# Performance work log

Measured on AMD Instinct MI355X. Metric: run time of the kernel, lower is better.

The kernel has to match this reference:

```python
import jax, jax.numpy as jnp
import numpy as np

K_NN = 32          # configs['k']
LEAKY_ALPHA = 0.2  # configs['alpha']
NHEADS = 8         # all heads share gat_W0/gat_a0 in the weights dict -> tiled output
NEG_INF = -9e15    # masked-softmax fill used by dense GAT


@jax.custom_vjp
def grad_reverse(x):
    # GradientReversalLayer: identity forward, negated gradient backward
    return x

def _gr_fwd(x):
    return x, None

def _gr_bwd(res, g):
    return (-g,)

grad_reverse.defvjp(_gr_fwd, _gr_bwd)


def setup_inputs() -> dict:
    key = jax.random.key(0)
    ks = jax.random.split(key, 11)
    N, D = 6144, 512           # N = (num_domains+1)*batch_size = 4*1536
    H1, H2, G = 256, 128, 64   # hidden_layers=[256,128], gat_hidden=[64]
    C, ND = 16, 3              # num_classes, num source-domain discriminators

    def xav(k, shape):
        limit = np.float32(np.sqrt(6.0 / (shape[0] + shape[1])) * 1.414)
        return jax.random.uniform(k, shape, jnp.float32, -limit, limit)

    return {
        "x": jax.random.normal(ks[0], (N, D), jnp.float32),
        "fc_W0": xav(ks[1], (D, H1)),
        "fc_b0": jax.random.normal(ks[2], (H1,), jnp.float32) * 0.01,
        "fc_W1": xav(ks[3], (H1, H2)),
        "fc_b1": jax.random.normal(ks[4], (H2,), jnp.float32) * 0.01,
        "gat_W": xav(ks[5], (H2, G)),
        "gat_a": jax.random.normal(ks[6], (2 * G, 1), jnp.float32) * 0.1,
        "cls_W": xav(ks[7], (NHEADS * G, C)),
        "cls_b": jax.random.normal(ks[8], (C,), jnp.float32) * 0.01,
        "dsc_W": jax.random.uniform(ks[9], (ND, NHEADS * G, 2), jnp.float32),
        "dsc_b": jax.random.uniform(ks[10], (ND, 2), jnp.float32),
    }


def reference(x, fc_W0, fc_b0, fc_W1, fc_b1, gat_W, gat_a, cls_W, cls_b, dsc_W, dsc_b):
    # --- feature extractor MLP (Linear 'fc' + relu), dropout=0 / eval mode ---
    h = jax.nn.relu(x @ fc_W0 + fc_b0)
    h = jax.nn.relu(h @ fc_W1 + fc_b1)          # [N, 128]
    n = h.shape[0]

    # --- AdjacencyLayer / DistanceLayer: kNN over pairwise L2 distances ---
    sq = jnp.sum(h * h, axis=1)
    d2 = sq[:, None] + sq[None, :] - 2.0 * (h @ h.T)      # [N, N] squared dists
    d2 = d2 + jnp.eye(n, dtype=h.dtype) * 1e9             # exclude self from kNN
    _, idx = jax.lax.top_k(-jax.lax.stop_gradient(d2), K_NN)  # [N, K]
    adj = jnp.zeros((n, n), h.dtype).at[jnp.arange(n)[:, None], idx].set(1.0)
    adj = adj + jnp.eye(n, dtype=h.dtype)                 # self loops

    # --- dense GraphAttentionLayer (single shared head, tiled nheads times) ---
    Wh = h @ gat_W                                        # [N, G]
    Gd = Wh.shape[1]
    f1 = Wh @ gat_a[:Gd]                                  # [N, 1]
    f2 = Wh @ gat_a[Gd:]                                  # [N, 1]
    e = jax.nn.leaky_relu(f1 + f2.T, LEAKY_ALPHA)         # [N, N]
    att = jax.nn.softmax(jnp.where(adj > 0, e, NEG_INF), axis=1)
    hp = jax.nn.elu(att @ Wh)                             # [N, G]
    gat_out = jnp.tile(hp, (1, NHEADS))                   # concat of shared heads

    # --- class head + domain discriminators behind gradient reversal ---
    cls_logits = gat_out @ cls_W + cls_b                  # [N, C]
    rev = grad_reverse(gat_out)
    dsc_logits = jnp.einsum('nd,kdo->nko', rev, dsc_W) + dsc_b  # [N, ND, 2]
    return jnp.concatenate([cls_logits, dsc_logits.reshape(n, -1)], axis=1)
```

## Files before the change

kernel.cpp:

```cpp
#include <hip/hip_runtime.h>
#include <float.h>

#define N_PTS 6144
#define D_IN  512
#define H1_DIM 256
#define H2_DIM 128
#define G_DIM  64
#define KNN    32
#define NOUT   22
#define NQ     (N_PTS / 4)

typedef short s8v __attribute__((ext_vector_type(8)));
typedef float f32x4 __attribute__((ext_vector_type(4)));
typedef unsigned u32x4 __attribute__((ext_vector_type(4)));
typedef unsigned short u16;
typedef unsigned short u16x4 __attribute__((ext_vector_type(4)));
typedef unsigned long long u64;

__device__ __forceinline__ u16 f2bf(float f) {
  unsigned u = __float_as_uint(f);
  u += 0x7FFFu + ((u >> 16) & 1u);
  return (u16)(u >> 16);
}
__device__ __forceinline__ float bf2f(u16 s) {
  return __uint_as_float(((unsigned)s) << 16);
}
__device__ __forceinline__ void split3(float v, u16& a0, u16& a1, u16& a2) {
  a0 = f2bf(v);
  float r1 = v - bf2f(a0);
  a1 = f2bf(r1);
  a2 = f2bf(r1 - bf2f(a1));
}
__device__ __forceinline__ unsigned sortkey(float f) {
  unsigned ub = __float_as_uint(f);
  return (ub & 0x80000000u) ? ~ub : (ub | 0x80000000u);
}

template<int BM, bool AF32, bool SPLITK, bool BIAS, bool RELU, bool WF32, bool WSPLIT>
__global__ __launch_bounds__(256, 4) void mfma_gemm(
    const void* __restrict__ A0any, const u16* __restrict__ A1_, const u16* __restrict__ A2_,
    const u16* __restrict__ B0_, const u16* __restrict__ B1_, const u16* __restrict__ B2_,
    const float* __restrict__ bias,
    float* __restrict__ Cf, u16* __restrict__ C0, u16* __restrict__ C1, u16* __restrict__ C2,
    int Ktot, int Ks, int ldC, size_t MN)
{
  const int MT = BM / 32, NT = 2;
  const int APL = BM * 32;
  const int BBASE = 3 * APL;
  __shared__ u16 lds[(BM + 64) * 32 * 3];

  const int t = threadIdx.x;
  const int lane = t & 63, wave = t >> 6;
  const int wm = wave >> 1, wn = wave & 1;
  const int m0 = blockIdx.y * BM, n0 = blockIdx.x * 64;
  const int kz = blockIdx.z * Ks;

  f32x4 acc[MT][NT] = {};

  const int pA = BM / 16;
  const int NC = 3 * pA + 12;

  for (int k0 = 0; k0 < Ks; k0 += 32) {
    if (k0) __syncthreads();
    const int kb = kz + k0;
    if (AF32) {
      const float* A = (const float*)A0any;
      #pragma unroll
      for (int c0 = 0; c0 < BM * 4; c0 += 256) {
        int c = c0 + t;
        int row = c >> 2, slot = c & 3;
        const float* g = A + (size_t)(m0 + row) * Ktot + kb + slot * 8;
        f32x4 fa = *(const f32x4*)g;
        f32x4 fb = *(const f32x4*)(g + 4);
        int dst = row * 32 + ((slot ^ ((row >> 1) & 3)) << 3);
        s8v v0, v1, v2;
        #pragma unroll
        for (int e = 0; e < 4; ++e) {
          u16 a0, a1, a2; split3(fa[e], a0, a1, a2);
          v0[e] = (short)a0; v1[e] = (short)a1; v2[e] = (short)a2;
        }
        #pragma unroll
        for (int e = 0; e < 4; ++e) {
          u16 a0, a1, a2; split3(fb[e], a0, a1, a2);
          v0[4 + e] = (short)a0; v1[4 + e] = (short)a1; v2[4 + e] = (short)a2;
        }
        *(s8v*)(lds + dst) = v0;
        *(s8v*)(lds + APL + dst) = v1;
        *(s8v*)(lds + 2 * APL + dst) = v2;
      }
      for (int c = wave; c < 12; c += 4) {
        int p = c >> 2, lc = c & 3;
        int row = lc * 16 + (lane >> 2);
        int srcslot = (lane & 3) ^ ((row >> 1) & 3);
        const u16* src = (p == 0) ? B0_ : (p == 1) ? B1_ : B2_;
        const u16* g = src + (size_t)(n0 + row) * Ktot + kb + srcslot * 8;
        __builtin_amdgcn_global_load_lds(
            (const __attribute__((address_space(1))) unsigned*)g,
            (__attribute__((address_space(3))) unsigned*)(lds + BBASE + p * 2048 + lc * 512),
            16, 0, 0);
      }
    } else {
      for (int c = wave; c < NC; c += 4) {
        const u16* src; int dstoff; int row0; int lc;
        if (c < 3 * pA) {
          int p = c / pA; lc = c % pA;
          src = (p == 0) ? (const u16*)A0any : (p == 1) ? A1_ : A2_;
          dstoff = p * APL + lc * 512;
          row0 = m0;
        } else {
          int cb = c - 3 * pA;
          int p = cb >> 2; lc = cb & 3;
          src = (p == 0) ? B0_ : (p == 1) ? B1_ : B2_;
          dstoff = BBASE + p * 2048 + lc * 512;
          row0 = n0;
        }
        int row = lc * 16 + (lane >> 2);
        int srcslot = (lane & 3) ^ ((row >> 1) & 3);
        const u16* g = src + (size_t)(row0 + row) * Ktot + kb + srcslot * 8;
        __builtin_amdgcn_global_load_lds(
            (const __attribute__((address_space(1))) unsigned*)g,
            (__attribute__((address_space(3))) unsigned*)(lds + dstoff),
            16, 0, 0);
      }
    }
    __syncthreads();

    s8v af[3][MT], bf[3][NT];
    #pragma unroll
    for (int mt = 0; mt < MT; ++mt) {
      int r = wm * (BM / 2) + mt * 16 + (lane & 15);
      int off = r * 32 + (((lane >> 4) ^ ((r >> 1) & 3)) << 3);
      #pragma unroll
      for (int p = 0; p < 3; ++p) af[p][mt] = *(const s8v*)(lds + p * APL + off);
    }
    #pragma unroll
    for (int nt = 0; nt < NT; ++nt) {
      int r = wn * 32 + nt * 16 + (lane & 15);
      int off = r * 32 + (((lane >> 4) ^ ((r >> 1) & 3)) << 3);
      #pragma unroll
      for (int p = 0; p < 3; ++p) bf[p][nt] = *(const s8v*)(lds + BBASE + p * 2048 + off);
    }
    #pragma unroll
    for (int mt = 0; mt < MT; ++mt)
      #pragma unroll
      for (int nt = 0; nt < NT; ++nt) {
        f32x4 a = acc[mt][nt];
        a = __builtin_amdgcn_mfma_f32_16x16x32_bf16(af[0][mt], bf[0][nt], a, 0, 0, 0);
        a = __builtin_amdgcn_mfma_f32_16x16x32_bf16(af[0][mt], bf[1][nt], a, 0, 0, 0);
        a = __builtin_amdgcn_mfma_f32_16x16x32_bf16(af[1][mt], bf[0][nt], a, 0, 0, 0);
        a = __builtin_amdgcn_mfma_f32_16x16x32_bf16(af[1][mt], bf[1][nt], a, 0, 0, 0);
        a = __builtin_amdgcn_mfma_f32_16x16x32_bf16(af[0][mt], bf[2][nt], a, 0, 0, 0);
        a = __builtin_amdgcn_mfma_f32_16x16x32_bf16(af[2][mt], bf[0][nt], a, 0, 0, 0);
        acc[mt][nt] = a;
      }
  }

  #pragma unroll
  for (int mt = 0; mt < MT; ++mt) {
    #pragma unroll
    for (int nt = 0; nt < NT; ++nt) {
      int col = n0 + wn * 32 + nt * 16 + (lane & 15);
      float bv = (BIAS && !SPLITK) ? bias[col] : 0.f;
      #pragma unroll
      for (int v = 0; v < 4; ++v) {
        int row = m0 + wm * (BM / 2) + mt * 16 + (lane >> 4) * 4 + v;
        float val = acc[mt][nt][v] + bv;
        size_t o = (size_t)row * ldC + col;
        if (SPLITK) {
          Cf[(size_t)blockIdx.z * MN + o] = val;
        } else {
          if (RELU) val = fmaxf(val, 0.f);
          if (WF32) Cf[o] = val;
          if (WSPLIT) {
            u16 a0, a1, a2; split3(val, a0, a1, a2);
            C0[o] = a0; C1[o] = a1; C2[o] = a2;
          }
        }
      }
    }
  }
}

__global__ __launch_bounds__(512, 4) void gram_symm(
    const u16* __restrict__ A0, const u16* __restrict__ A1, const u16* __restrict__ A2,
    const float* __restrict__ sq, u16* __restrict__ Ck, u16* __restrict__ Qm, int ldC)
{
  if ((int)blockIdx.x < (int)blockIdx.y) return;
  const int MT = 4, NT = 2;
  __shared__ u16 lds[2 * 128 * 32 * 3];

  const int t = threadIdx.x;
  const int lane = t & 63, wave = t >> 6;
  const int wm = wave >> 2, wn = wave & 3;
  const int m0 = blockIdx.y * 128, n0 = blockIdx.x * 128;
  const bool mirror = (int)blockIdx.x > (int)blockIdx.y;

  f32x4 acc[MT][NT] = {};

  for (int k0 = 0; k0 < H2_DIM; k0 += 32) {
    if (k0) __syncthreads();
    for (int c = wave; c < 48; c += 8) {
      int half = c >= 24;
      int cb = half ? c - 24 : c;
      int p = cb >> 3, lc = cb & 7;
      const u16* src = (p == 0) ? A0 : (p == 1) ? A1 : A2;
      int dstoff = half * 12288 + p * 4096 + lc * 512;
      int row0 = half ? n0 : m0;
      int row = lc * 16 + (lane >> 2);
      int srcslot = (lane & 3) ^ ((row >> 1) & 3);
      const u16* g = src + (size_t)(row0 + row) * H2_DIM + k0 + srcslot * 8;
      __builtin_amdgcn_global_load_lds(
          (const __attribute__((address_space(1))) unsigned*)g,
          (__attribute__((address_space(3))) unsigned*)(lds + dstoff),
          16, 0, 0);
    }
    __syncthreads();

    s8v af[3][MT], bf[3][NT];
    #pragma unroll
    for (int mt = 0; mt < MT; ++mt) {
      int r = wm * 64 + mt * 16 + (lane & 15);
      int off = r * 32 + (((lane >> 4) ^ ((r >> 1) & 3)) << 3);
      #pragma unroll
      for (int p = 0; p < 3; ++p) af[p][mt] = *(const s8v*)(lds + p * 4096 + off);
    }
    #pragma unroll
    for (int nt = 0; nt < NT; ++nt) {
      int r = wn * 32 + nt * 16 + (lane & 15);
      int off = r * 32 + (((lane >> 4) ^ ((r >> 1) & 3)) << 3);
      #pragma unroll
      for (int p = 0; p < 3; ++p) bf[p][nt] = *(const s8v*)(lds + 12288 + p * 4096 + off);
    }
    #pragma unroll
    for (int mt = 0; mt < MT; ++mt)
      #pragma unroll
      for (int nt = 0; nt < NT; ++nt) {
        f32x4 a = acc[mt][nt];
        a = __builtin_amdgcn_mfma_f32_16x16x32_bf16(af[0][mt], bf[0][nt], a, 0, 0, 0);
        a = __builtin_amdgcn_mfma_f32_16x16x32_bf16(af[0][mt], bf[1][nt], a, 0, 0, 0);
        a = __builtin_amdgcn_mfma_f32_16x16x32_bf16(af[1][mt], bf[0][nt], a, 0, 0, 0);
        a = __builtin_amdgcn_mfma_f32_16x16x32_bf16(af[1][mt], bf[1][nt], a, 0, 0, 0);
        a = __builtin_amdgcn_mfma_f32_16x16x32_bf16(af[0][mt], bf[2][nt], a, 0, 0, 0);
        a = __builtin_amdgcn_mfma_f32_16x16x32_bf16(af[2][mt], bf[0][nt], a, 0, 0, 0);
        acc[mt][nt] = a;
      }
  }

  unsigned mk32[MT][NT][2];
  __syncthreads();
  u16* stD = lds;
  #pragma unroll
  for (int mt = 0; mt < MT; ++mt) {
    #pragma unroll
    for (int nt = 0; nt < NT; ++nt) {
      int cl = wn * 32 + nt * 16 + (lane & 15);
      float sqc = sq[n0 + cl];
      #pragma unroll
      for (int v = 0; v < 4; ++v) {
        int rl = wm * 64 + mt * 16 + (lane >> 4) * 4 + v;
        float val = acc[mt][nt][v];
        float f = fmaf(-2.f, val, sqc);
        unsigned uu = sortkey(f);
        if (m0 + rl == n0 + cl) uu = 0xFFFFFFFFu;
        stD[rl * 136 + cl] = (u16)(uu >> 16);
        if (mirror) {
          unsigned km = sortkey(fmaf(-2.f, val, sq[m0 + rl])) >> 16;
          if (v & 1) mk32[mt][nt][v >> 1] |= km << 16;
          else       mk32[mt][nt][v >> 1] = km;
        }
      }
    }
  }
  __syncthreads();
  for (int e = t; e < 128 * 16; e += 512) {
    int row = e >> 4, ch = e & 15;
    u32x4 vv = *(const u32x4*)(stD + row * 136 + ch * 8);
    *(u32x4*)(Ck + (size_t)(m0 + row) * ldC + n0 + ch * 8) = vv;
  }
  for (int e = t; e < 128 * 32; e += 512) {
    int row = e >> 5, qg = e & 31;
    const u16* p = stD + row * 136 + qg * 4;
    u16 a = p[0] < p[1] ? p[0] : p[1];
    u16 b = p[2] < p[3] ? p[2] : p[3];
    Qm[(size_t)(m0 + row) * NQ + (n0 >> 2) + qg] = a < b ? a : b;
  }
  if (mirror) {
    __syncthreads();
    u16* stM = lds;
    #pragma unroll
    for (int mt = 0; mt < MT; ++mt) {
      #pragma unroll
      for (int nt = 0; nt < NT; ++nt) {
        int cl = wn * 32 + nt * 16 + (lane & 15);
        #pragma unroll
        for (int v = 0; v < 4; ++v) {
          int rl = wm * 64 + mt * 16 + (lane >> 4) * 4 + v;
          unsigned km = (v & 1) ? (mk32[mt][nt][v >> 1] >> 16)
                                : (mk32[mt][nt][v >> 1] & 0xFFFFu);
          stM[cl * 136 + rl] = (u16)km;
        }
      }
    }
    __syncthreads();
    for (int e = t; e < 128 * 16; e += 512) {
      int row = e >> 4, ch = e & 15;
      u32x4 vv = *(const u32x4*)(stM + row * 136 + ch * 8);
      *(u32x4*)(Ck + (size_t)(n0 + row) * ldC + m0 + ch * 8) = vv;
    }
    for (int e = t; e < 128 * 32; e += 512) {
      int row = e >> 5, qg = e & 31;
      const u16* p = stM + row * 136 + qg * 4;
      u16 a = p[0] < p[1] ? p[0] : p[1];
      u16 b = p[2] < p[3] ? p[2] : p[3];
      Qm[(size_t)(n0 + row) * NQ + (m0 >> 2) + qg] = a < b ? a : b;
    }
  }
}

template<int S, bool BIAS, bool RELU, bool WF32, bool WSPLIT>
__global__ void combine(const float* __restrict__ P, const float* __restrict__ bias,
                        size_t MN, int Ncols,
                        float* __restrict__ Cf, u16* __restrict__ C0,
                        u16* __restrict__ C1, u16* __restrict__ C2)
{
  size_t idx = ((size_t)blockIdx.x * 256 + threadIdx.x) * 4;
  if (idx >= MN) return;
  f32x4 s = *(const f32x4*)(P + idx);
  #pragma unroll
  for (int z = 1; z < S; ++z) s += *(const f32x4*)(P + (size_t)z * MN + idx);
  int n = (int)(idx % (size_t)Ncols);
  #pragma unroll
  for (int e = 0; e < 4; ++e) {
    float v = s[e] + (BIAS ? bias[n + e] : 0.f);
    if (RELU) v = fmaxf(v, 0.f);
    if (WF32) Cf[idx + e] = v;
    if (WSPLIT) {
      u16 a0, a1, a2; split3(v, a0, a1, a2);
      C0[idx + e] = a0; C1[idx + e] = a1; C2[idx + e] = a2;
    }
  }
}

__global__ void prep_all(const float* __restrict__ W0, u16* __restrict__ a0,
                         u16* __restrict__ a1, u16* __restrict__ a2,
                         const float* __restrict__ W1, u16* __restrict__ b0,
                         u16* __restrict__ b1, u16* __restrict__ b2,
                         const float* __restrict__ gW, u16* __restrict__ c0,
                         u16* __restrict__ c1, u16* __restrict__ c2,
                         const float* __restrict__ cW, const float* __restrict__ cb,
                         const float* __restrict__ dW, const float* __restrict__ db,
                         float* __restrict__ Wc, float* __restrict__ bc)
{
  int id = blockIdx.x * 256 + threadIdx.x;
  const int S0 = D_IN * H1_DIM, S1 = H1_DIM * H2_DIM, S2 = H2_DIM * G_DIM;
  const int SW = S0 + S1 + S2;
  if (id < SW) {
    const float* W; u16 *p0, *p1, *p2; int K, N;
    if (id < S0)           { W = W0; p0 = a0; p1 = a1; p2 = a2; K = D_IN;   N = H1_DIM; }
    else if (id < S0 + S1) { id -= S0; W = W1; p0 = b0; p1 = b1; p2 = b2; K = H1_DIM; N = H2_DIM; }
    else                   { id -= S0 + S1; W = gW; p0 = c0; p1 = c1; p2 = c2; K = H2_DIM; N = G_DIM; }
    int k = id / N, n = id % N;
    u16 x0, x1, x2;
    split3(W[id], x0, x1, x2);
    size_t o = (size_t)n * K + k;
    p0[o] = x0; p1[o] = x1; p2[o] = x2;
    return;
  }
  id -= SW;
  if (id < 64 * NOUT) {
    int g = id / NOUT, c = id % NOUT;
    float s = 0.f;
    if (c < 16) {
      for (int r = 0; r < 8; ++r) s += cW[(r * 64 + g) * 16 + c];
    } else {
      int k = (c - 16) >> 1, o = (c - 16) & 1;
      for (int r = 0; r < 8; ++r) s += dW[k * 1024 + (r * 64 + g) * 2 + o];
    }
    Wc[id] = s;
    if (g == 0) bc[c] = (c < 16) ? cb[c] : db[c - 16];
  }
}

__global__ void row_stats(const float* __restrict__ h, const float* __restrict__ Wh,
                          const float* __restrict__ ga, float* __restrict__ sq,
                          float* __restrict__ f1, float* __restrict__ f2)
{
  int i = blockIdx.x * 256 + threadIdx.x;
  const float* hr = h + (size_t)i * H2_DIM;
  float s = 0.f;
  for (int k = 0; k < H2_DIM; ++k) { float v = hr[k]; s = fmaf(v, v, s); }
  sq[i] = s;
  const float* wr = Wh + (size_t)i * G_DIM;
  float a = 0.f, b = 0.f;
  for (int g = 0; g < G_DIM; ++g) {
    float w = wr[g];
    a = fmaf(w, ga[g], a);
    b = fmaf(w, ga[G_DIM + g], b);
  }
  f1[i] = a; f2[i] = b;
}

__global__ __launch_bounds__(256) void topk_att(const u16* __restrict__ Sb,
    const u16* __restrict__ Qm,
    const float* __restrict__ f1, const float* __restrict__ f2,
    const float* __restrict__ Wh, const float* __restrict__ Wc, const float* __restrict__ bc,
    const float* __restrict__ sq, const float* __restrict__ hF,
    float* __restrict__ out, int m0, int nrows)
{
  const int t = threadIdx.x;
  const int lane = t & 63, wv = t >> 6;
  const int row4 = (nrows - 4 - blockIdx.x * 4) + wv;
  const int i = m0 + row4;
  const u16* Srow = Sb + (size_t)row4 * N_PTS;
  const u16* Qrow = Qm + (size_t)row4 * NQ;

  __shared__ float WcL[64 * NOUT];
  __shared__ unsigned candS[4][384];
  __shared__ u16 tieS[4][128];
  __shared__ float hiL[4][128];
  __shared__ int neighS[4][33];
  __shared__ float attS[4][33];
  __shared__ float hpfS[4][64];

  for (int idx = t; idx < 64 * NOUT; idx += 256) WcL[idx] = Wc[idx];
  __syncthreads();

  hiL[wv][lane]      = hF[(size_t)i * H2_DIM + lane];
  hiL[wv][64 + lane] = hF[(size_t)i * H2_DIM + 64 + lane];

  unsigned q[24];
  #pragma unroll
  for (int g = 0; g < 6; ++g) {
    u16x4 v = *(const u16x4*)(Qrow + (g << 8) + (lane << 2));
    #pragma unroll
    for (int e = 0; e < 4; ++e) q[g * 4 + e] = (unsigned)v[e];
  }
  #define QI(s) (((s >> 2) << 8) + (lane << 2) + (s & 3))

  unsigned lmin = q[0];
  #pragma unroll
  for (int c = 1; c < 24; ++c) lmin = q[c] < lmin ? q[c] : lmin;

  unsigned mnl = lmin, mxl = lmin;
  #pragma unroll
  for (int off = 32; off > 0; off >>= 1) {
    unsigned o1 = __shfl_xor(mnl, off); mnl = o1 < mnl ? o1 : mnl;
    unsigned o2 = __shfl_xor(mxl, off); mxl = o2 > mxl ? o2 : mxl;
  }

  long long lo = (long long)mnl - 1, hi = (long long)mxl;
  while (hi - lo > 1) {
    long long span = hi - lo;
    unsigned m1 = (unsigned)(lo + (span >> 2));
    unsigned m2 = (unsigned)(lo + (span >> 1));
    unsigned m3 = (unsigned)(hi - (span >> 2));
    int c1 = 0, c2 = 0, c3 = 0;
    #pragma unroll
    for (int c = 0; c < 24; ++c) {
      c1 += (q[c] <= m1);
      c2 += (q[c] <= m2);
      c3 += (q[c] <= m3);
    }
    #pragma unroll
    for (int off = 32; off > 0; off >>= 1) {
      c1 += __shfl_xor(c1, off);
      c2 += __shfl_xor(c2, off);
      c3 += __shfl_xor(c3, off);
    }
    if (c1 >= KNN)       { hi = m1; }
    else if (c2 >= KNN)  { lo = m1; hi = m2; }
    else if (c3 >= KNN)  { lo = m2; hi = m3; }
    else                 { lo = m3; }
  }
  const unsigned Q = (unsigned)hi;

  #pragma unroll
  for (int s = 0; s < 6; ++s) candS[wv][lane + s * 64] = 0xFFFFFFFFu;
  const u64 below = (lane == 0) ? 0ull : (~0ull >> (64 - lane));
  int qcnt = 0;
  #pragma unroll
  for (int s = 0; s < 24; ++s) {
    bool act = (q[s] <= Q);
    u64 mask = __ballot(act);
    if (act) {
      int pos = qcnt + (int)__popcll(mask & below);
      if (pos < 96) {
        int qi = QI(s);
        u16x4 v = *(const u16x4*)(Srow + (qi << 2));
        #pragma unroll
        for (int e = 0; e < 4; ++e) {
          int j = (qi << 2) + e;
          candS[wv][pos * 4 + e] = ((unsigned)v[e] << 13) | (unsigned)j;
        }
      }
    }
    qcnt += (int)__popcll(mask);
  }

  unsigned ck[6];
  #pragma unroll
  for (int s = 0; s < 6; ++s) ck[s] = candS[wv][lane + s * 64];

  unsigned kmn = 0x10000u, kmx = 0u;
  #pragma unroll
  for (int s = 0; s < 6; ++s) {
    unsigned k = ck[s] >> 13;
    if (k <= 0xFFFFu) {
      kmn = k < kmn ? k : kmn;
      kmx = k > kmx ? k : kmx;
    }
  }
  #pragma unroll
  for (int off = 32; off > 0; off >>= 1) {
    unsigned o1 = __shfl_xor(kmn, off); kmn = o1 < kmn ? o1 : kmn;
    unsigned o2 = __shfl_xor(kmx, off); kmx = o2 > kmx ? o2 : kmx;
  }

  lo = (long long)kmn - 1; hi = (long long)kmx;
  while (hi - lo > 1) {
    long long span = hi - lo;
    unsigned m1 = (unsigned)(lo + (span >> 2));
    unsigned m2 = (unsigned)(lo + (span >> 1));
    unsigned m3 = (unsigned)(hi - (span >> 2));
    int c1 = 0, c2 = 0, c3 = 0;
    #pragma unroll
    for (int s = 0; s < 6; ++s) {
      unsigned k = ck[s] >> 13;
      c1 += (k <= m1);
      c2 += (k <= m2);
      c3 += (k <= m3);
    }
    #pragma unroll
    for (int off = 32; off > 0; off >>= 1) {
      c1 += __shfl_xor(c1, off);
      c2 += __shfl_xor(c2, off);
      c3 += __shfl_xor(c3, off);
    }
    if (c1 >= KNN)       { hi = m1; }
    else if (c2 >= KNN)  { lo = m1; hi = m2; }
    else if (c3 >= KNN)  { lo = m2; hi = m3; }
    else                 { lo = m3; }
  }
  const unsigned T = (unsigned)hi;

  int sA = 0, sB = 0;
  #pragma unroll
  for (int s = 0; s < 6; ++s) {
    unsigned k = ck[s] >> 13;
    bool strict = (k < T);
    u64 ms = __ballot(strict);
    if (strict) {
      int pos = sA + (int)__popcll(ms & below);
      if (pos < 32) neighS[wv][pos] = (int)(ck[s] & 0x1FFFu);
    }
    sA += (int)__popcll(ms);
    bool tie = (k == T);
    u64 mt2 = __ballot(tie);
    if (tie) {
      int pos = sB + (int)__popcll(mt2 & below);
      if (pos < 128) tieS[wv][pos] = (u16)(ck[s] & 0x1FFFu);
    }
    sB += (int)__popcll(mt2);
  }
  if (sB > 128) sB = 128;
  const int need = KNN - sA;

  if (sB == need) {
    if (lane < need) neighS[wv][sA + lane] = tieS[wv][lane];
  } else {
    u64 r0 = ~0ull, r1 = ~0ull;
    const float* hi0 = &hiL[wv][0];
    #pragma unroll
    for (int half = 0; half < 2; ++half) {
      int e = lane + half * 64;
      if (e < sB) {
        int j = tieS[wv][e];
        const float* hj = hF + (size_t)j * H2_DIM;
        float d0 = 0.f, d1 = 0.f, d2 = 0.f, d3 = 0.f;
        for (int d = 0; d < H2_DIM; d += 16) {
          f32x4 a0 = *(const f32x4*)(hi0 + d);
          f32x4 b0 = *(const f32x4*)(hj + d);
          f32x4 a1 = *(const f32x4*)(hi0 + d + 4);
          f32x4 b1 = *(const f32x4*)(hj + d + 4);
          f32x4 a2 = *(const f32x4*)(hi0 + d + 8);
          f32x4 b2 = *(const f32x4*)(hj + d + 8);
          f32x4 a3 = *(const f32x4*)(hi0 + d + 12);
          f32x4 b3 = *(const f32x4*)(hj + d + 12);
          d0 = fmaf(a0[0], b0[0], fmaf(a0[1], b0[1], fmaf(a0[2], b0[2], fmaf(a0[3], b0[3], d0))));
          d1 = fmaf(a1[0], b1[0], fmaf(a1[1], b1[1], fmaf(a1[2], b1[2], fmaf(a1[3], b1[3], d1))));
          d2 = fmaf(a2[0], b2[0], fmaf(a2[1], b2[1], fmaf(a2[2], b2[2], fmaf(a2[3], b2[3], d2))));
          d3 = fmaf(a3[0], b3[0], fmaf(a3[1], b3[1], fmaf(a3[2], b3[2], fmaf(a3[3], b3[3], d3))));
        }
        float dot = (d0 + d1) + (d2 + d3);
        float f = fmaf(-2.f, dot, sq[j]);
        u64 rk = ((u64)sortkey(f) << 13) | (unsigned)j;
        if (half == 0) r0 = rk; else r1 = rk;
      }
    }

    candS[wv][lane] = (unsigned)(r0 >> 32); candS[wv][64 + lane] = (unsigned)r0;
    candS[wv][128 + lane] = (unsigned)(r1 >> 32); candS[wv][192 + lane] = (unsigned)r1;
    u64 v0 = ((u64)candS[wv][(2 * lane) >= 64 ? 128 + (2 * lane - 64) : 2 * lane] << 32)
           | candS[wv][(2 * lane) >= 64 ? 192 + (2 * lane - 64) : 64 + 2 * lane];
    u64 v1 = ((u64)candS[wv][(2 * lane + 1) >= 64 ? 128 + (2 * lane + 1 - 64) : 2 * lane + 1] << 32)
           | candS[wv][(2 * lane + 1) >= 64 ? 192 + (2 * lane + 1 - 64) : 64 + 2 * lane + 1];
    const int e0 = 2 * lane, e1 = e0 + 1;
    for (int k = 2; k <= 128; k <<= 1) {
      for (int j = k >> 1; j >= 2; j >>= 1) {
        int half = j >> 1;
        u64 o0 = __shfl_xor(v0, half);
        u64 o1 = __shfl_xor(v1, half);
        bool up0 = ((e0 & k) == 0) == ((e0 & j) == 0);
        bool up1 = ((e1 & k) == 0) == ((e1 & j) == 0);
        v0 = up0 ? (v0 < o0 ? v0 : o0) : (v0 > o0 ? v0 : o0);
        v1 = up1 ? (v1 < o1 ? v1 : o1) : (v1 > o1 ? v1 : o1);
      }
      bool asc = ((e0 & k) == 0);
      u64 a = v0 < v1 ? v0 : v1, b = v0 < v1 ? v1 : v0;
      v0 = asc ? a : b;
      v1 = asc ? b : a;
    }
    if (e0 < need) neighS[wv][sA + e0] = (int)(v0 & 0x1FFFu);
    if (e1 < need) neighS[wv][sA + e1] = (int)(v1 & 0x1FFFu);
  }
  if (lane == 0) neighS[wv][32] = i;

  {
    float e = -FLT_MAX;
    if (lane < 33) {
      float raw = f1[i] + f2[neighS[wv][lane]];
      e = raw > 0.f ? raw : 0.2f * raw;
    }
    float mx = e;
    #pragma unroll
    for (int off = 32; off > 0; off >>= 1) mx = fmaxf(mx, __shfl_xor(mx, off));
    float ex = (lane < 33) ? expf(e - mx) : 0.f;
    float sm = ex;
    #pragma unroll
    for (int off = 32; off > 0; off >>= 1) sm += __shfl_xor(sm, off);
    if (lane < 33) attS[wv][lane] = ex / sm;
  }

  {
    float s = 0.f;
    for (int m = 0; m < 33; ++m)
      s = fmaf(attS[wv][m], Wh[(size_t)neighS[wv][m] * G_DIM + lane], s);
    hpfS[wv][lane] = s > 0.f ? s : expm1f(s);
  }

  if (lane < NOUT) {
    float o = bc[lane];
    for (int g = 0; g < 64; ++g) o = fmaf(hpfS[wv][g], WcL[g * NOUT + lane], o);
    out[(size_t)i * NOUT + lane] = o;
  }
}

extern "C" void kernel_launch(void* const* d_in, const int* in_sizes, int n_in,
                              void* d_out, int out_size, void* d_ws, size_t ws_size,
                              hipStream_t stream)
{
  const float* x  = (const float*)d_in[0];
  const float* W0 = (const float*)d_in[1];
  const float* b0 = (const float*)d_in[2];
  const float* W1 = (const float*)d_in[3];
  const float* b1 = (const float*)d_in[4];
  const float* gW = (const float*)d_in[5];
  const float* ga = (const float*)d_in[6];
  const float* cW = (const float*)d_in[7];
  const float* cb = (const float*)d_in[8];
  const float* dW = (const float*)d_in[9];
  const float* db = (const float*)d_in[10];
  float* out = (float*)d_out;

  char* base = (char*)d_ws;
  char* w = base;
  auto alloc = [&](size_t bytes) { char* p = w; w += (bytes + 255) & ~(size_t)255; return p; };
  u16 *W0p[3], *W1p[3], *gWp[3], *h1p[3], *hp[3];
  for (int p = 0; p < 3; ++p) W0p[p] = (u16*)alloc((size_t)D_IN * H1_DIM * 2);
  for (int p = 0; p < 3; ++p) W1p[p] = (u16*)alloc((size_t)H1_DIM * H2_DIM * 2);
  for (int p = 0; p < 3; ++p) gWp[p] = (u16*)alloc((size_t)H2_DIM * G_DIM * 2);
  for (int p = 0; p < 3; ++p) h1p[p] = (u16*)alloc((size_t)N_PTS * H1_DIM * 2);
  for (int p = 0; p < 3; ++p) hp[p]  = (u16*)alloc((size_t)N_PTS * H2_DIM * 2);
  float* hF  = (float*)alloc((size_t)N_PTS * H2_DIM * 4);
  float* WhF = (float*)alloc((size_t)N_PTS * G_DIM * 4);
  float* sqv = (float*)alloc(N_PTS * 4);
  float* f1v = (float*)alloc(N_PTS * 4);
  float* f2v = (float*)alloc(N_PTS * 4);
  float* Wc  = (float*)alloc(64 * NOUT * 4);
  float* bc  = (float*)alloc(64 * 4);
  u16* Qm    = (u16*)alloc((size_t)N_PTS * NQ * 2);

  char* pbase = w;
  const size_t MN1 = (size_t)N_PTS * H1_DIM;
  const size_t MN2 = (size_t)N_PTS * H2_DIM;
  const size_t MN3 = (size_t)N_PTS * G_DIM;
  float* P1 = (float*)alloc(2 * MN1 * 4);
  float* P2 = (float*)alloc(4 * MN2 * 4);
  float* P3 = (float*)alloc(4 * MN3 * 4);
  u16* Sb = (u16*)pbase;

  const int TS = D_IN * H1_DIM + H1_DIM * H2_DIM + H2_DIM * G_DIM + 64 * NOUT;
  prep_all<<<(TS + 255) / 256, 256, 0, stream>>>(
      W0, W0p[0], W0p[1], W0p[2], W1, W1p[0], W1p[1], W1p[2], gW, gWp[0], gWp[1], gWp[2],
      cW, cb, dW, db, Wc, bc);

  mfma_gemm<64, true, true, false, false, false, false>
      <<<dim3(H1_DIM / 64, N_PTS / 64, 2), 256, 0, stream>>>(
      x, nullptr, nullptr, W0p[0], W0p[1], W0p[2], nullptr,
      P1, nullptr, nullptr, nullptr, D_IN, D_IN / 2, H1_DIM, MN1);
  combine<2, true, true, false, true><<<(int)(MN1 / 1024), 256, 0, stream>>>(
      P1, b0, MN1, H1_DIM, nullptr, h1p[0], h1p[1], h1p[2]);

  mfma_gemm<64, false, true, false, false, false, false>
      <<<dim3(H2_DIM / 64, N_PTS / 64, 4), 256, 0, stream>>>(
      h1p[0], h1p[1], h1p[2], W1p[0], W1p[1], W1p[2], nullptr,
      P2, nullptr, nullptr, nullptr, H1_DIM, H1_DIM / 4, H2_DIM, MN2);
  combine<4, true, true, true, true><<<(int)(MN2 / 1024), 256, 0, stream>>>(
      P2, b1, MN2, H2_DIM, hF, hp[0], hp[1], hp[2]);

  mfma_gemm<64, false, true, false, false, false, false>
      <<<dim3(G_DIM / 64, N_PTS / 64, 4), 256, 0, stream>>>(
      hp[0], hp[1], hp[2], gWp[0], gWp[1], gWp[2], nullptr,
      P3, nullptr, nullptr, nullptr, H2_DIM, H2_DIM / 4, G_DIM, MN3);
  combine<4, false, false, true, false><<<(int)(MN3 / 1024), 256, 0, stream>>>(
      P3, nullptr, MN3, G_DIM, WhF, nullptr, nullptr, nullptr);

  row_stats<<<N_PTS / 256, 256, 0, stream>>>(hF, WhF, ga, sqv, f1v, f2v);

  gram_symm<<<dim3(N_PTS / 128, N_PTS / 128), 512, 0, stream>>>(
      hp[0], hp[1], hp[2], sqv, Sb, Qm, N_PTS);
  topk_att<<<N_PTS / 4, 256, 0, stream>>>(Sb, Qm, f1v, f2v, WhF, Wc, bc, sqv, hF, out, 0, N_PTS);
}
```

Measured before the change: 162.7 us.

## Process two rows per wavefront in top-k attention and split first GEMM four ways

The top-k/attention kernel now has each wavefront handle two rows at once. Their threshold searches, candidate gathers, reductions and output projections are interleaved so independent shuffles and memory loads overlap, and the Wc tile load is amortized over twice as many rows. Grid size is halved and shared memory per block doubles. Separately, the first MLP GEMM uses split-K of 4 instead of 2 for more blocks, at the cost of a larger partial buffer and more combine traffic.

New measurement: 163.0 us. Within noise of the previous version (+0.2%).

```diff
diff --git a/kernel.cpp b/kernel.cpp
--- a/kernel.cpp
+++ b/kernel.cpp
@@ -409,172 +409,246 @@
 {
   const int t = threadIdx.x;
   const int lane = t & 63, wv = t >> 6;
-  const int row4 = (nrows - 4 - blockIdx.x * 4) + wv;
-  const int i = m0 + row4;
-  const u16* Srow = Sb + (size_t)row4 * N_PTS;
-  const u16* Qrow = Qm + (size_t)row4 * NQ;
+  const int rbase = (nrows - 8 - blockIdx.x * 8) + wv * 2;
+  const int i0 = m0 + rbase, i1 = i0 + 1;
+  const u16* SrowA = Sb + (size_t)rbase * N_PTS;
+  const u16* SrowB = SrowA + N_PTS;
+  const u16* QrowA = Qm + (size_t)rbase * NQ;
+  const u16* QrowB = QrowA + NQ;
 
   __shared__ float WcL[64 * NOUT];
-  __shared__ unsigned candS[4][384];
-  __shared__ u16 tieS[4][128];
-  __shared__ float hiL[4][128];
-  __shared__ int neighS[4][33];
-  __shared__ float attS[4][33];
-  __shared__ float hpfS[4][64];
+  __shared__ unsigned candS[4][2][384];
+  __shared__ u16 tieS[4][2][128];
+  __shared__ float hiL[4][2][128];
+  __shared__ int neighS[4][2][33];
+  __shared__ float attS[4][2][33];
+  __shared__ float hpfS[4][2][64];
 
   for (int idx = t; idx < 64 * NOUT; idx += 256) WcL[idx] = Wc[idx];
   __syncthreads();
 
-  hiL[wv][lane]      = hF[(size_t)i * H2_DIM + lane];
-  hiL[wv][64 + lane] = hF[(size_t)i * H2_DIM + 64 + lane];
-
-  unsigned q[24];
+  hiL[wv][0][lane]      = hF[(size_t)i0 * H2_DIM + lane];
+  hiL[wv][0][64 + lane] = hF[(size_t)i0 * H2_DIM + 64 + lane];
+  hiL[wv][1][lane]      = hF[(size_t)i1 * H2_DIM + lane];
+  hiL[wv][1][64 + lane] = hF[(size_t)i1 * H2_DIM + 64 + lane];
+
+  unsigned q[2][24];
   #pragma unroll
   for (int g = 0; g < 6; ++g) {
-    u16x4 v = *(const u16x4*)(Qrow + (g << 8) + (lane << 2));
-    #pragma unroll
-    for (int e = 0; e < 4; ++e) q[g * 4 + e] = (unsigned)v[e];
-  }
-  #define QI(s) (((s >> 2) << 8) + (lane << 2) + (s & 3))
-
-  unsigned lmin = q[0];
-  #pragma unroll
-  for (int c = 1; c < 24; ++c) lmin = q[c] < lmin ? q[c] : lmin;
-
-  unsigned mnl = lmin, mxl = lmin;
+    u16x4 vA = *(const u16x4*)(QrowA + (g << 8) + (lane << 2));
+    u16x4 vB = *(const u16x4*)(QrowB + (g << 8) + (lane << 2));
+    #pragma unroll
+    for (int e = 0; e < 4; ++e) {
+      q[0][g * 4 + e] = (unsigned)vA[e];
+      q[1][g * 4 + e] = (unsigned)vB[e];
+    }
+  }
+  #define QI(s) (((s >> 2) << 8) + (lane << 2) + ((s) & 3))
+
+  unsigned mn[2], mx[2];
+  #pragma unroll
+  for (int r = 0; r < 2; ++r) {
+    unsigned lmin = q[r][0];
+    #pragma unroll
+    for (int c = 1; c < 24; ++c) lmin = q[r][c] < lmin ? q[r][c] : lmin;
+    mn[r] = lmin; mx[r] = lmin;
+  }
   #pragma unroll
   for (int off = 32; off > 0; off >>= 1) {
-    unsigned o1 = __shfl_xor(mnl, off); mnl = o1 < mnl ? o1 : mnl;
-    unsigned o2 = __shfl_xor(mxl, off); mxl = o2 > mxl ? o2 : mxl;
-  }
-
-  long long lo = (long long)mnl - 1, hi = (long long)mxl;
-  while (hi - lo > 1) {
-    long long span = hi - lo;
-    unsigned m1 = (unsigned)(lo + (span >> 2));
-    unsigned m2 = (unsigned)(lo + (span >> 1));
-    unsigned m3 = (unsigned)(hi - (span >> 2));
-    int c1 = 0, c2 = 0, c3 = 0;
+    #pragma unroll
+    for (int r = 0; r < 2; ++r) {
+      unsigned o1 = __shfl_xor(mn[r], off); mn[r] = o1 < mn[r] ? o1 : mn[r];
+      unsigned o2 = __shfl_xor(mx[r], off); mx[r] = o2 > mx[r] ? o2 : mx[r];
+    }
+  }
+
+  long long lo[2], hi[2];
+  #pragma unroll
+  for (int r = 0; r < 2; ++r) { lo[r] = (long long)mn[r] - 1; hi[r] = (long long)mx[r]; }
+  while ((hi[0] - lo[0] > 1) || (hi[1] - lo[1] > 1)) {
+    unsigned mm[2][3];
+    int cnt[2][3] = {};
+    #pragma unroll
+    for (int r = 0; r < 2; ++r) {
+      long long span = hi[r] - lo[r];
+      mm[r][0] = (unsigned)(lo[r] + (span >> 2));
+      mm[r][1] = (unsigned)(lo[r] + (span >> 1));
+      mm[r][2] = (unsigned)(hi[r] - (span >> 2));
+    }
     #pragma unroll
     for (int c = 0; c < 24; ++c) {
-      c1 += (q[c] <= m1);
-      c2 += (q[c] <= m2);
-      c3 += (q[c] <= m3);
+      #pragma unroll
+      for (int r = 0; r < 2; ++r) {
+        cnt[r][0] += (q[r][c] <= mm[r][0]);
+        cnt[r][1] += (q[r][c] <= mm[r][1]);
+        cnt[r][2] += (q[r][c] <= mm[r][2]);
+      }
     }
     #pragma unroll
     for (int off = 32; off > 0; off >>= 1) {
-      c1 += __shfl_xor(c1, off);
-      c2 += __shfl_xor(c2, off);
-      c3 += __shfl_xor(c3, off);
-    }
-    if (c1 >= KNN)       { hi = m1; }
-    else if (c2 >= KNN)  { lo = m1; hi = m2; }
-    else if (c3 >= KNN)  { lo = m2; hi = m3; }
-    else                 { lo = m3; }
-  }
-  const unsigned Q = (unsigned)hi;
-
-  #pragma unroll
-  for (int s = 0; s < 6; ++s) candS[wv][lane + s * 64] = 0xFFFFFFFFu;
+      #pragma unroll
+      for (int r = 0; r < 2; ++r) {
+        cnt[r][0] += __shfl_xor(cnt[r][0], off);
+        cnt[r][1] += __shfl_xor(cnt[r][1], off);
+        cnt[r][2] += __shfl_xor(cnt[r][2], off);
+      }
+    }
+    #pragma unroll
+    for (int r = 0; r < 2; ++r) {
+      if (hi[r] - lo[r] > 1) {
+        if (cnt[r][0] >= KNN)      { hi[r] = mm[r][0]; }
+        else if (cnt[r][1] >= KNN) { lo[r] = mm[r][0]; hi[r] = mm[r][1]; }
+        else if (cnt[r][2] >= KNN) { lo[r] = mm[r][1]; hi[r] = mm[r][2]; }
+        else                       { lo[r] = mm[r][2]; }
+      }
+    }
+  }
+  const unsigned Qv0 = (unsigned)hi[0], Qv1 = (unsigned)hi[1];
+
+  #pragma unroll
+  for (int s = 0; s < 6; ++s) {
+    candS[wv][0][lane + s * 64] = 0xFFFFFFFFu;
+    candS[wv][1][lane + s * 64] = 0xFFFFFFFFu;
+  }
   const u64 below = (lane == 0) ? 0ull : (~0ull >> (64 - lane));
-  int qcnt = 0;
+  int qcA = 0, qcB = 0;
   #pragma unroll
   for (int s = 0; s < 24; ++s) {
-    bool act = (q[s] <= Q);
-    u64 mask = __ballot(act);
-    if (act) {
-      int pos = qcnt + (int)__popcll(mask & below);
+    bool aA = (q[0][s] <= Qv0);
+    u64 mA = __ballot(aA);
+    if (aA) {
+      int pos = qcA + (int)__popcll(mA & below);
       if (pos < 96) {
         int qi = QI(s);
-        u16x4 v = *(const u16x4*)(Srow + (qi << 2));
+        u16x4 v = *(const u16x4*)(SrowA + (qi << 2));
         #pragma unroll
-        for (int e = 0; e < 4; ++e) {
-          int j = (qi << 2) + e;
-          candS[wv][pos * 4 + e] = ((unsigned)v[e] << 13) | (unsigned)j;
-        }
-      }
-    }
-    qcnt += (int)__popcll(mask);
-  }
-
-  unsigned ck[6];
-  #pragma unroll
-  for (int s = 0; s < 6; ++s) ck[s] = candS[wv][lane + s * 64];
-
-  unsigned kmn = 0x10000u, kmx = 0u;
+        for (int e = 0; e < 4; ++e)
+          candS[wv][0][pos * 4 + e] = ((unsigned)v[e] << 13) | (unsigned)((qi << 2) + e);
+      }
+    }
+    qcA += (int)__popcll(mA);
+    bool aB = (q[1][s] <= Qv1);
+    u64 mB = __ballot(aB);
+    if (aB) {
+      int pos = qcB + (int)__popcll(mB & below);
+      if (pos < 96) {
+        int qi = QI(s);
+        u16x4 v = *(const u16x4*)(SrowB + (qi << 2));
+        #pragma unroll
+        for (int e = 0; e < 4; ++e)
+          candS[wv][1][pos * 4 + e] = ((unsigned)v[e] << 13) | (unsigned)((qi << 2) + e);
+      }
+    }
+    qcB += (int)__popcll(mB);
+  }
+
+  unsigned ck[2][6];
   #pragma unroll
   for (int s = 0; s < 6; ++s) {
-    unsigned k = ck[s] >> 13;
-    if (k <= 0xFFFFu) {
-      kmn = k < kmn ? k : kmn;
-      kmx = k > kmx ? k : kmx;
+    ck[0][s] = candS[wv][0][lane + s * 64];
+    ck[1][s] = candS[wv][1][lane + s * 64];
+  }
+
+  unsigned kmn[2] = {0x10000u, 0x10000u}, kmx[2] = {0u, 0u};
+  #pragma unroll
+  for (int s = 0; s < 6; ++s) {
+    #pragma unroll
+    for (int r = 0; r < 2; ++r) {
+      unsigned k = ck[r][s] >> 13;
+      if (k <= 0xFFFFu) {
+        kmn[r] = k < kmn[r] ? k : kmn[r];
+        kmx[r] = k > kmx[r] ? k : kmx[r];
+      }
     }
   }
   #pragma unroll
   for (int off = 32; off > 0; off >>= 1) {
-    unsigned o1 = __shfl_xor(kmn, off); kmn = o1 < kmn ? o1 : kmn;
-    unsigned o2 = __shfl_xor(kmx, off); kmx = o2 > kmx ? o2 : kmx;
-  }
-
-  lo = (long long)kmn - 1; hi = (long long)kmx;
-  while (hi - lo > 1) {
-    long long span = hi - lo;
-    unsigned m1 = (unsigned)(lo + (span >> 2));
-    unsigned m2 = (unsigned)(lo + (span >> 1));
-    unsigned m3 = (unsigned)(hi - (span >> 2));
-    int c1 = 0, c2 = 0, c3 = 0;
+    #pragma unroll
+    for (int r = 0; r < 2; ++r) {
+      unsigned o1 = __shfl_xor(kmn[r], off); kmn[r] = o1 < kmn[r] ? o1 : kmn[r];
+      unsigned o2 = __shfl_xor(kmx[r], off); kmx[r] = o2 > kmx[r] ? o2 : kmx[r];
+    }
+  }
+
+  #pragma unroll
+  for (int r = 0; r < 2; ++r) { lo[r] = (long long)kmn[r] - 1; hi[r] = (long long)kmx[r]; }
+  while ((hi[0] - lo[0] > 1) || (hi[1] - lo[1] > 1)) {
+    unsigned mm[2][3];
+    int cnt[2][3] = {};
+    #pragma unroll
+    for (int r = 0; r < 2; ++r) {
+      long long span = hi[r] - lo[r];
+      mm[r][0] = (unsigned)(lo[r] + (span >> 2));
+      mm[r][1] = (unsigned)(lo[r] + (span >> 1));
+      mm[r][2] = (unsigned)(hi[r] - (span >> 2));
+    }
     #pragma unroll
     for (int s = 0; s < 6; ++s) {
-      unsigned k = ck[s] >> 13;
-      c1 += (k <= m1);
-      c2 += (k <= m2);
-      c3 += (k <= m3);
+      #pragma unroll
+      for (int r = 0; r < 2; ++r) {
+        unsigned k = ck[r][s] >> 13;
+        cnt[r][0] += (k <= mm[r][0]);
+        cnt[r][1] += (k <= mm[r][1]);
+        cnt[r][2] += (k <= mm[r][2]);
+      }
     }
     #pragma unroll
     for (int off = 32; off > 0; off >>= 1) {
-      c1 += __shfl_xor(c1, off);
-      c2 += __shfl_xor(c2, off);
-      c3 += __shfl_xor(c3, off);
-    }
-    if (c1 >= KNN)       { hi = m1; }
-    else if (c2 >= KNN)  { lo = m1; hi = m2; }
-    else if (c3 >= KNN)  { lo = m2; hi = m3; }
-    else                 { lo = m3; }
-  }
-  const unsigned T = (unsigned)hi;
-
-  int sA = 0, sB = 0;
+      #pragma unroll
+      for (int r = 0; r < 2; ++r) {
+        cnt[r][0] += __shfl_xor(cnt[r][0], off);
+        cnt[r][1] += __shfl_xor(cnt[r][1], off);
+        cnt[r][2] += __shfl_xor(cnt[r][2], off);
+      }
+    }
+    #pragma unroll
+    for (int r = 0; r < 2; ++r) {
+      if (hi[r] - lo[r] > 1) {
+        if (cnt[r][0] >= KNN)      { hi[r] = mm[r][0]; }
+        else if (cnt[r][1] >= KNN) { lo[r] = mm[r][0]; hi[r] = mm[r][1]; }
+        else if (cnt[r][2] >= KNN) { lo[r] = mm[r][1]; hi[r] = mm[r][2]; }
+        else                       { lo[r] = mm[r][2]; }
+      }
+    }
+  }
+  const unsigned T[2] = {(unsigned)hi[0], (unsigned)hi[1]};
+
+  int sA[2] = {0, 0}, sB[2] = {0, 0};
   #pragma unroll
   for (int s = 0; s < 6; ++s) {
-    unsigned k = ck[s] >> 13;
-    bool strict = (k < T);
-    u64 ms = __ballot(strict);
-    if (strict) {
-      int pos = sA + (int)__popcll(ms & below);
-      if (pos < 32) neighS[wv][pos] = (int)(ck[s] & 0x1FFFu);
-    }
-    sA += (int)__popcll(ms);
-    bool tie = (k == T);
-    u64 mt2 = __ballot(tie);
-    if (tie) {
-      int pos = sB + (int)__popcll(mt2 & below);
-      if (pos < 128) tieS[wv][pos] = (u16)(ck[s] & 0x1FFFu);
-    }
-    sB += (int)__popcll(mt2);
-  }
-  if (sB > 128) sB = 128;
-  const int need = KNN - sA;
-
-  if (sB == need) {
-    if (lane < need) neighS[wv][sA + lane] = tieS[wv][lane];
-  } else {
-    u64 r0 = ~0ull, r1 = ~0ull;
-    const float* hi0 = &hiL[wv][0];
-    #pragma unroll
-    for (int half = 0; half < 2; ++half) {
+    #pragma unroll
+    for (int r = 0; r < 2; ++r) {
+      unsigned k = ck[r][s] >> 13;
+      bool strict = (k < T[r]);
+      u64 ms = __ballot(strict);
+      if (strict) {
+        int pos = sA[r] + (int)__popcll(ms & below);
+        if (pos < 32) neighS[wv][r][pos] = (int)(ck[r][s] & 0x1FFFu);
+      }
+      sA[r] += (int)__popcll(ms);
+      bool tie = (k == T[r]);
+      u64 mt2 = __ballot(tie);
+      if (tie) {
+        int pos = sB[r] + (int)__popcll(mt2 & below);
+        if (pos < 128) tieS[wv][r][pos] = (u16)(ck[r][s] & 0x1FFFu);
+      }
+      sB[r] += (int)__popcll(mt2);
+    }
+  }
+  #pragma unroll
+  for (int r = 0; r < 2; ++r) if (sB[r] > 128) sB[r] = 128;
+  const int need[2] = {KNN - sA[0], KNN - sA[1]};
+  const bool doref[2] = {sB[0] != need[0], sB[1] != need[1]};
+
+  u64 rk[2][2] = {{~0ull, ~0ull}, {~0ull, ~0ull}};
+  #pragma unroll
+  for (int half = 0; half < 2; ++half) {
+    #pragma unroll
+    for (int r = 0; r < 2; ++r) {
       int e = lane + half * 64;
-      if (e < sB) {
-        int j = tieS[wv][e];
+      if (doref[r] && e < sB[r]) {
+        int j = tieS[wv][r][e];
+        const float* hi0 = &hiL[wv][r][0];
         const float* hj = hF + (size_t)j * H2_DIM;
         float d0 = 0.f, d1 = 0.f, d2 = 0.f, d3 = 0.f;
         for (int d = 0; d < H2_DIM; d += 16) {
@@ -593,65 +667,91 @@
         }
         float dot = (d0 + d1) + (d2 + d3);
         float f = fmaf(-2.f, dot, sq[j]);
-        u64 rk = ((u64)sortkey(f) << 13) | (unsigned)j;
-        if (half == 0) r0 = rk; else r1 = rk;
-      }
-    }
-
-    candS[wv][lane] = (unsigned)(r0 >> 32); candS[wv][64 + lane] = (unsigned)r0;
-    candS[wv][128 + lane] = (unsigned)(r1 >> 32); candS[wv][192 + lane] = (unsigned)r1;
-    u64 v0 = ((u64)candS[wv][(2 * lane) >= 64 ? 128 + (2 * lane - 64) : 2 * lane] << 32)
-           | candS[wv][(2 * lane) >= 64 ? 192 + (2 * lane - 64) : 64 + 2 * lane];
-    u64 v1 = ((u64)candS[wv][(2 * lane + 1) >= 64 ? 128 + (2 * lane + 1 - 64) : 2 * lane + 1] << 32)
-           | candS[wv][(2 * lane + 1) >= 64 ? 192 + (2 * lane + 1 - 64) : 64 + 2 * lane + 1];
-    const int e0 = 2 * lane, e1 = e0 + 1;
-    for (int k = 2; k <= 128; k <<= 1) {
-      for (int j = k >> 1; j >= 2; j >>= 1) {
-        int half = j >> 1;
-        u64 o0 = __shfl_xor(v0, half);
-        u64 o1 = __shfl_xor(v1, half);
-        bool up0 = ((e0 & k) == 0) == ((e0 & j) == 0);
-        bool up1 = ((e1 & k) == 0) == ((e1 & j) == 0);
-        v0 = up0 ? (v0 < o0 ? v0 : o0) : (v0 > o0 ? v0 : o0);
-        v1 = up1 ? (v1 < o1 ? v1 : o1) : (v1 > o1 ? v1 : o1);
-      }
-      bool asc = ((e0 & k) == 0);
-      u64 a = v0 < v1 ? v0 : v1, b = v0 < v1 ? v1 : v0;
-      v0 = asc ? a : b;
-      v1 = asc ? b : a;
-    }
-    if (e0 < need) neighS[wv][sA + e0] = (int)(v0 & 0x1FFFu);
-    if (e1 < need) neighS[wv][sA + e1] = (int)(v1 & 0x1FFFu);
-  }
-  if (lane == 0) neighS[wv][32] = i;
+        rk[r][half] = ((u64)sortkey(f) << 13) | (unsigned)j;
+      }
+    }
+  }
+
+  #pragma unroll
+  for (int r = 0; r < 2; ++r) {
+    if (!doref[r]) {
+      if (lane < need[r]) neighS[wv][r][sA[r] + lane] = tieS[wv][r][lane];
+    } else {
+      candS[wv][r][lane]       = (unsigned)(rk[r][0] >> 32);
+      candS[wv][r][64 + lane]  = (unsigned)rk[r][0];
+      candS[wv][r][128 + lane] = (unsigned)(rk[r][1] >> 32);
+      candS[wv][r][192 + lane] = (unsigned)rk[r][1];
+      u64 v0 = ((u64)candS[wv][r][(2 * lane) >= 64 ? 128 + (2 * lane - 64) : 2 * lane] << 32)
+             | candS[wv][r][(2 * lane) >= 64 ? 192 + (2 * lane - 64) : 64 + 2 * lane];
+      u64 v1 = ((u64)candS[wv][r][(2 * lane + 1) >= 64 ? 128 + (2 * lane + 1 - 64) : 2 * lane + 1] << 32)
+             | candS[wv][r][(2 * lane + 1) >= 64 ? 192 + (2 * lane + 1 - 64) : 64 + 2 * lane + 1];
+      const int e0 = 2 * lane, e1 = e0 + 1;
+      for (int k = 2; k <= 128; k <<= 1) {
+        for (int j = k >> 1; j >= 2; j >>= 1) {
+          int half = j >> 1;
+          u64 o0 = __shfl_xor(v0, half);
+          u64 o1 = __shfl_xor(v1, half);
+          bool up0 = ((e0 & k) == 0) == ((e0 & j) == 0);
+          bool up1 = ((e1 & k) == 0) == ((e1 & j) == 0);
+          v0 = up0 ? (v0 < o0 ? v0 : o0) : (v0 > o0 ? v0 : o0);
+          v1 = up1 ? (v1 < o1 ? v1 : o1) : (v1 > o1 ? v1 : o1);
+        }
+        bool asc = ((e0 & k) == 0);
+        u64 a = v0 < v1 ? v0 : v1, b = v0 < v1 ? v1 : v0;
+        v0 = asc ? a : b;
+        v1 = asc ? b : a;
+      }
+      if (e0 < need[r]) neighS[wv][r][sA[r] + e0] = (int)(v0 & 0x1FFFu);
+      if (e1 < need[r]) neighS[wv][r][sA[r] + e1] = (int)(v1 & 0x1FFFu);
+    }
+    if (lane == 0) neighS[wv][r][32] = (r == 0) ? i0 : i1;
+  }
+
+  float eA = -FLT_MAX, eB = -FLT_MAX;
+  if (lane < 33) {
+    float rawA = f1[i0] + f2[neighS[wv][0][lane]];
+    float rawB = f1[i1] + f2[neighS[wv][1][lane]];
+    eA = rawA > 0.f ? rawA : 0.2f * rawA;
+    eB = rawB > 0.f ? rawB : 0.2f * rawB;
+  }
+  float mxA = eA, mxB = eB;
+  #pragma unroll
+  for (int off = 32; off > 0; off >>= 1) {
+    mxA = fmaxf(mxA, __shfl_xor(mxA, off));
+    mxB = fmaxf(mxB, __shfl_xor(mxB, off));
+  }
+  float exA = (lane < 33) ? expf(eA - mxA) : 0.f;
+  float exB = (lane < 33) ? expf(eB - mxB) : 0.f;
+  float smA = exA, smB = exB;
+  #pragma unroll
+  for (int off = 32; off > 0; off >>= 1) {
+    smA += __shfl_xor(smA, off);
+    smB += __shfl_xor(smB, off);
+  }
+  if (lane < 33) {
+    attS[wv][0][lane] = exA / smA;
+    attS[wv][1][lane] = exB / smB;
+  }
 
   {
-    float e = -FLT_MAX;
-    if (lane < 33) {
-      float raw = f1[i] + f2[neighS[wv][lane]];
-      e = raw > 0.f ? raw : 0.2f * raw;
-    }
-    float mx = e;
-    #pragma unroll
-    for (int off = 32; off > 0; off >>= 1) mx = fmaxf(mx, __shfl_xor(mx, off));
-    float ex = (lane < 33) ? expf(e - mx) : 0.f;
-    float sm = ex;
-    #pragma unroll
-    for (int off = 32; off > 0; off >>= 1) sm += __shfl_xor(sm, off);
-    if (lane < 33) attS[wv][lane] = ex / sm;
-  }
-
-  {
-    float s = 0.f;
-    for (int m = 0; m < 33; ++m)
-      s = fmaf(attS[wv][m], Wh[(size_t)neighS[wv][m] * G_DIM + lane], s);
-    hpfS[wv][lane] = s > 0.f ? s : expm1f(s);
+    float s0 = 0.f, s1 = 0.f;
+    for (int m = 0; m < 33; ++m) {
+      s0 = fmaf(attS[wv][0][m], Wh[(size_t)neighS[wv][0][m] * G_DIM + lane], s0);
+      s1 = fmaf(attS[wv][1][m], Wh[(size_t)neighS[wv][1][m] * G_DIM + lane], s1);
+    }
+    hpfS[wv][0][lane] = s0 > 0.f ? s0 : expm1f(s0);
+    hpfS[wv][1][lane] = s1 > 0.f ? s1 : expm1f(s1);
   }
 
   if (lane < NOUT) {
-    float o = bc[lane];
-    for (int g = 0; g < 64; ++g) o = fmaf(hpfS[wv][g], WcL[g * NOUT + lane], o);
-    out[(size_t)i * NOUT + lane] = o;
+    float o0 = bc[lane], o1 = bc[lane];
+    for (int g = 0; g < 64; ++g) {
+      float wgt = WcL[g * NOUT + lane];
+      o0 = fmaf(hpfS[wv][0][g], wgt, o0);
+      o1 = fmaf(hpfS[wv][1][g], wgt, o1);
+    }
+    out[(size_t)i0 * NOUT + lane] = o0;
+    out[(size_t)i1 * NOUT + lane] = o1;
   }
 }
 
@@ -694,7 +794,7 @@
   const size_t MN1 = (size_t)N_PTS * H1_DIM;
   const size_t MN2 = (size_t)N_PTS * H2_DIM;
   const size_t MN3 = (size_t)N_PTS * G_DIM;
-  float* P1 = (float*)alloc(2 * MN1 * 4);
+  float* P1 = (float*)alloc(4 * MN1 * 4);
   float* P2 = (float*)alloc(4 * MN2 * 4);
   float* P3 = (float*)alloc(4 * MN3 * 4);
   u16* Sb = (u16*)pbase;
@@ -705,10 +805,10 @@
       cW, cb, dW, db, Wc, bc);
 
   mfma_gemm<64, true, true, false, false, false, false>
-      <<<dim3(H1_DIM / 64, N_PTS / 64, 2), 256, 0, stream>>>(
+      <<<dim3(H1_DIM / 64, N_PTS / 64, 4), 256, 0, stream>>>(
       x, nullptr, nullptr, W0p[0], W0p[1], W0p[2], nullptr,
-      P1, nullptr, nullptr, nullptr, D_IN, D_IN / 2, H1_DIM, MN1);
-  combine<2, true, true, false, true><<<(int)(MN1 / 1024), 256, 0, stream>>>(
+      P1, nullptr, nullptr, nullptr, D_IN, D_IN / 4, H1_DIM, MN1);
+  combine<4, true, true, false, true><<<(int)(MN1 / 1024), 256, 0, stream>>>(
       P1, b0, MN1, H1_DIM, nullptr, h1p[0], h1p[1], h1p[2]);
 
   mfma_gemm<64, false, true, false, false, false, false>
@@ -729,5 +829,5 @@
 
   gram_symm<<<dim3(N_PTS / 128, N_PTS / 128), 512, 0, stream>>>(
       hp[0], hp[1], hp[2], sqv, Sb, Qm, N_PTS);
-  topk_att<<<N_PTS / 4, 256, 0, stream>>>(Sb, Qm, f1v, f2v, WhF, Wc, bc, sqv, hF, out, 0, N_PTS);
-}
+  topk_att<<<N_PTS / 8, 256, 0, stream>>>(Sb, Qm, f1v, f2v, WhF, Wc, bc, sqv, hF, out, 0, N_PTS);
+}
```
